# Optimization experiments

Measured on AMD Instinct MI355X. Metric: run time of the kernel, lower is better.

Reference implementation:

```python
import jax, jax.numpy as jnp
import numpy as np

EMBED_DIM = 2048
N_HEADS = 16
HEAD_DIM = EMBED_DIM // N_HEADS


def setup_inputs() -> dict:
    key = jax.random.key(0)
    ks = jax.random.split(key, 5)
    s = 1.0 / np.sqrt(EMBED_DIM)
    x = jax.random.normal(ks[0], (2, 2048, EMBED_DIM), dtype=jnp.float32)
    W_qkv = jax.random.uniform(ks[1], (EMBED_DIM, 3 * EMBED_DIM), jnp.float32, -s, s)
    b_qkv = jax.random.uniform(ks[2], (3 * EMBED_DIM,), jnp.float32, -s, s)
    W_out = jax.random.uniform(ks[3], (EMBED_DIM, EMBED_DIM), jnp.float32, -s, s)
    b_out = jax.random.uniform(ks[4], (EMBED_DIM,), jnp.float32, -s, s)
    return {"x": x, "W_qkv": W_qkv, "b_qkv": b_qkv, "W_out": W_out, "b_out": b_out}


def reference(x, W_qkv, b_qkv, W_out, b_out):
    batch, seq_len, _ = x.shape
    qkv = jnp.einsum('bsd,de->bse', x, W_qkv) + b_qkv
    q, k, v = jnp.split(qkv, 3, axis=-1)
    # [b, h, s, hd]
    def heads(t):
        return t.reshape(batch, seq_len, N_HEADS, HEAD_DIM).transpose(0, 2, 1, 3)
    q, k, v = heads(q), heads(k), heads(v)
    scale = 1.0 / np.sqrt(HEAD_DIM)
    scores = jnp.einsum('bhqd,bhkd->bhqk', q, k) * scale  # [b,h,s,s]
    causal = jnp.tril(jnp.ones((seq_len, seq_len), dtype=bool))
    scores = jnp.where(causal, scores, -jnp.inf)
    attn = jax.nn.softmax(scores, axis=-1)
    out = jnp.einsum('bhqk,bhkd->bhqd', attn, v)
    out = out.transpose(0, 2, 1, 3).reshape(batch, seq_len, EMBED_DIM)
    return jnp.einsum('bsd,de->bse', out, W_out) + b_out
```

## Files before the change

### kernel.cpp

```cpp
#include <hip/hip_runtime.h>
#include <hip/hip_bf16.h>

#define EMBED  2048
#define SEQ    2048
#define BATCH  2
#define NHEADS 16
#define HDIM   128
#define QKVC   (3*EMBED)
#define ROWS   (BATCH*SEQ)

typedef __attribute__((ext_vector_type(8))) short bf16x8;
typedef __attribute__((ext_vector_type(4))) float f32x4;
typedef __attribute__((ext_vector_type(16))) float f32x16;

typedef const __attribute__((address_space(1))) void* gptr1_t;
typedef __attribute__((address_space(3))) void* lptr3_t;

__device__ __forceinline__ void gld16(const unsigned short* g, unsigned short* l) {
  __builtin_amdgcn_global_load_lds((gptr1_t)g, (lptr3_t)l, 16, 0, 0);
}

__device__ __forceinline__ unsigned short f2bf(float f) {
  unsigned int x = __float_as_uint(f);
  unsigned int r = (x + 0x7fffu + ((x >> 16) & 1u)) >> 16;
  return (unsigned short)r;
}

__global__ __launch_bounds__(256)
void prep_kernel(const float* __restrict__ x,
                 const float* __restrict__ Wqkv,
                 const float* __restrict__ Wout,
                 unsigned short* __restrict__ xb,
                 unsigned short* __restrict__ wqkvT,
                 unsigned short* __restrict__ woutT) {
  __shared__ float tile[32][33];
  const int bid = blockIdx.x;
  if (bid < 8192) {
    int i = bid * 256 + threadIdx.x;
    float4 v = reinterpret_cast<const float4*>(x)[i];
    ushort4 o;
    o.x = f2bf(v.x); o.y = f2bf(v.y); o.z = f2bf(v.z); o.w = f2bf(v.w);
    reinterpret_cast<ushort4*>(xb)[i] = o;
    return;
  }
  const float* in; unsigned short* out; int C, bx, by;
  if (bid < 8192 + 12288) {
    int j = bid - 8192;  bx = j % 192; by = j / 192;  in = Wqkv; out = wqkvT; C = QKVC;
  } else {
    int j = bid - 20480; bx = j % 64;  by = j / 64;   in = Wout; out = woutT; C = EMBED;
  }
  const int R = EMBED;
  int tx = threadIdx.x & 31, ty = threadIdx.x >> 5;
  int c0 = bx * 32, r0 = by * 32;
  #pragma unroll
  for (int i = 0; i < 32; i += 8)
    tile[ty + i][tx] = in[(size_t)(r0 + ty + i) * C + c0 + tx];
  __syncthreads();
  #pragma unroll
  for (int i = 0; i < 32; i += 8)
    out[(size_t)(c0 + ty + i) * R + r0 + tx] = f2bf(tile[tx][ty + i]);
}

template<int MODE>
__global__ __launch_bounds__(256)
void gemm_kernel(const unsigned short* __restrict__ A,
                 const unsigned short* __restrict__ BT,
                 const float* __restrict__ bias,
                 unsigned short* __restrict__ outb,
                 unsigned short* __restrict__ vt,
                 float* __restrict__ outf,
                 int M, int N, int K) {
  __shared__ unsigned short As[2 * 128 * 32];
  __shared__ unsigned short Bs[2 * 128 * 32];
  const int t = threadIdx.x;
  const int lane = t & 63, wave = t >> 6;
  const int l31 = lane & 31, hl = lane >> 5;
  const int wm = wave >> 1, wn = wave & 1;
  const int m0 = blockIdx.y * 128, n0 = blockIdx.x * 128;

  f32x16 acc[2][2] = {};

  int aoff[2][4], boff[2][4];
  #pragma unroll
  for (int i = 0; i < 2; ++i) {
    int m = wm * 64 + i * 32 + l31;
    int pm = ((m >> 2) ^ m) & 3;
    int n = wn * 64 + i * 32 + l31;
    int pn = ((n >> 2) ^ n) & 3;
    #pragma unroll
    for (int s4 = 0; s4 < 4; ++s4) {
      int st = s4 >> 1, c = (s4 & 1) * 2 + hl;
      aoff[i][s4] = st * 4096 + (m * 4 + (c ^ pm)) * 8;
      boff[i][s4] = st * 4096 + (n * 4 + (c ^ pn)) * 8;
    }
  }
  int ldso[4];
  const unsigned short* Ag[4];
  const unsigned short* Bg[4];
  #pragma unroll
  for (int i = 0; i < 4; ++i) {
    int cc = i * 256 + t;
    int st = cc >> 9, w = cc & 511;
    int r = w >> 2, s = w & 3;
    int d = s ^ (((r >> 2) ^ r) & 3);
    ldso[i] = st * 4096 + w * 8;
    Ag[i] = A  + (size_t)(m0 + r) * K + st * 32 + d * 8;
    Bg[i] = BT + (size_t)(n0 + r) * K + st * 32 + d * 8;
  }

  for (int k0 = 0; k0 < K; k0 += 64) {
    #pragma unroll
    for (int i = 0; i < 4; ++i) gld16(Ag[i] + k0, &As[ldso[i]]);
    #pragma unroll
    for (int i = 0; i < 4; ++i) gld16(Bg[i] + k0, &Bs[ldso[i]]);
    __syncthreads();
    #pragma unroll
    for (int s4 = 0; s4 < 4; ++s4) {
      bf16x8 a0 = *(const bf16x8*)&As[aoff[0][s4]];
      bf16x8 a1 = *(const bf16x8*)&As[aoff[1][s4]];
      bf16x8 b0 = *(const bf16x8*)&Bs[boff[0][s4]];
      bf16x8 b1 = *(const bf16x8*)&Bs[boff[1][s4]];
      acc[0][0] = __builtin_amdgcn_mfma_f32_32x32x16_bf16(a0, b0, acc[0][0], 0, 0, 0);
      acc[0][1] = __builtin_amdgcn_mfma_f32_32x32x16_bf16(a0, b1, acc[0][1], 0, 0, 0);
      acc[1][0] = __builtin_amdgcn_mfma_f32_32x32x16_bf16(a1, b0, acc[1][0], 0, 0, 0);
      acc[1][1] = __builtin_amdgcn_mfma_f32_32x32x16_bf16(a1, b1, acc[1][1], 0, 0, 0);
    }
    __syncthreads();
  }

  #pragma unroll
  for (int i = 0; i < 2; ++i) {
    int rowb = m0 + wm * 64 + i * 32 + 4 * hl;
    #pragma unroll
    for (int j = 0; j < 2; ++j) {
      int col = n0 + wn * 64 + j * 32 + l31;
      float bv = bias[col];
      if (MODE == 1) {
        #pragma unroll
        for (int g = 0; g < 4; ++g)
          #pragma unroll
          for (int rr = 0; rr < 4; ++rr)
            outf[(size_t)(rowb + 8 * g + rr) * N + col] = acc[i][j][4 * g + rr] + bv;
      } else {
        int hd = col;
        int b = rowb >> 11;
        int sbase = rowb & 2047;
        #pragma unroll
        for (int g = 0; g < 4; ++g) {
          ushort4 w;
          w.x = f2bf(acc[i][j][4 * g + 0] + bv);
          w.y = f2bf(acc[i][j][4 * g + 1] + bv);
          w.z = f2bf(acc[i][j][4 * g + 2] + bv);
          w.w = f2bf(acc[i][j][4 * g + 3] + bv);
          *(ushort4*)&vt[(((size_t)(b << 11) + hd) << 11) + sbase + 8 * g] = w;
        }
      }
    }
  }
}

#define FENCE256 asm volatile("" ::: "memory")
#define BAR256 do { FENCE256; __builtin_amdgcn_s_barrier(); FENCE256; } while (0)

#define STAGE_A256(BUF, H, KT) do { if ((KT) < NT) { \
    gld16(Asrc[0] + (H)*128*K + (KT)*64, &As[BUF][(H)*8192 + sdst0]); \
    gld16(Asrc[1] + (H)*128*K + (KT)*64, &As[BUF][(H)*8192 + sdst1]); } } while (0)
#define STAGE_B256(BUF, H, KT) do { if ((KT) < NT) { \
    gld16(Bsrc[0] + (H)*128*K + (KT)*64, &Bs[BUF][(H)*8192 + sdst0]); \
    gld16(Bsrc[1] + (H)*128*K + (KT)*64, &Bs[BUF][(H)*8192 + sdst1]); } } while (0)

#define READ_A256(BUF, MH) do { _Pragma("unroll") \
  for (int mf = 0; mf < 4; ++mf) { \
    av[mf][0] = *(const bf16x8*)&As[BUF][arow0 + (MH)*4096 + mf*1024 + ck0]; \
    av[mf][1] = *(const bf16x8*)&As[BUF][arow0 + (MH)*4096 + mf*1024 + ck1]; } } while (0)
#define READ_B256(BUF, NH, DST) do { _Pragma("unroll") \
  for (int nf = 0; nf < 2; ++nf) { \
    DST[nf][0] = *(const bf16x8*)&Bs[BUF][brow0 + (NH)*2048 + nf*1024 + ck0]; \
    DST[nf][1] = *(const bf16x8*)&Bs[BUF][brow0 + (NH)*2048 + nf*1024 + ck1]; } } while (0)

#define MFMA_Q256(MH, NH, B_) do { \
  __builtin_amdgcn_s_setprio(1); \
  _Pragma("unroll") \
  for (int mf = 0; mf < 4; ++mf) { \
    _Pragma("unroll") \
    for (int nf = 0; nf < 2; ++nf) { \
      f32x4 c = acc[(MH)*4 + mf][(NH)*2 + nf]; \
      c = __builtin_amdgcn_mfma_f32_16x16x32_bf16(av[mf][0], B_[nf][0], c, 0, 0, 0); \
      c = __builtin_amdgcn_mfma_f32_16x16x32_bf16(av[mf][1], B_[nf][1], c, 0, 0, 0); \
      acc[(MH)*4 + mf][(NH)*2 + nf] = c; } } \
  __builtin_amdgcn_s_setprio(0); } while (0)

#define VMCNT256(LAST) do { \
  if (LAST) asm volatile("s_waitcnt vmcnt(0)" ::: "memory"); \
  else      asm volatile("s_waitcnt vmcnt(4)" ::: "memory"); } while (0)

__global__ __launch_bounds__(512, 2)
void gemm256_kernel(const unsigned short* __restrict__ A,
                    const unsigned short* __restrict__ BT,
                    const float* __restrict__ bias,
                    unsigned short* __restrict__ outb,
                    unsigned short* __restrict__ vt,
                    int M, int N, int K) {
  __shared__ __align__(16) unsigned short As[2][16384];
  __shared__ __align__(16) unsigned short Bs[2][16384];
  const int t = threadIdx.x;
  const int lane = t & 63, wave = t >> 6;
  const int l16 = lane & 15, quad = (lane >> 4) & 3;
  const int wm = wave >> 2, wn = wave & 3;

  const int nwg = (int)gridDim.x;
  int swz = (int)blockIdx.x;
  if ((nwg & 7) == 0) swz = (swz & 7) * (nwg >> 3) + (swz >> 3);
  const int ntiles = N >> 8;
  const int mt = swz / ntiles, nt = swz % ntiles;
  const int m0 = mt << 8, n0 = nt << 8;

  const int NT = K >> 6;
  const int NI = NT >> 1;

  f32x4 acc[8][4] = {};
  bf16x8 av[4][2], bv0[2][2], bv1[2][2];

  const unsigned short* Asrc[2];
  const unsigned short* Bsrc[2];
  int sdst0, sdst1;
  {
    int cc0 = t, cc1 = 512 + t;
    int r0 = cc0 >> 3, c0 = cc0 & 7;
    int r1 = cc1 >> 3, c1 = cc1 & 7;
    Asrc[0] = A  + (size_t)(m0 + r0) * K + ((c0 ^ (r0 & 7)) << 3);
    Asrc[1] = A  + (size_t)(m0 + r1) * K + ((c1 ^ (r1 & 7)) << 3);
    Bsrc[0] = BT + (size_t)(n0 + r0) * K + ((c0 ^ (r0 & 7)) << 3);
    Bsrc[1] = BT + (size_t)(n0 + r1) * K + ((c1 ^ (r1 & 7)) << 3);
    sdst0 = cc0 << 3;
    sdst1 = cc1 << 3;
  }

  const int ck0 = ((quad) ^ (l16 & 7)) << 3;
  const int ck1 = ((4 + quad) ^ (l16 & 7)) << 3;
  const int arow0 = (wm * 128 + l16) * 64;
  const int brow0 = (wn * 64 + l16) * 64;

  STAGE_A256(0, 0, 0); STAGE_A256(0, 1, 0);
  STAGE_B256(0, 0, 0); STAGE_B256(0, 1, 0);
  STAGE_B256(1, 0, 1); STAGE_B256(1, 1, 1);
  asm volatile("s_waitcnt vmcnt(4)" ::: "memory");
  BAR256;

  for (int it = 0; it < NI; ++it) {
    const int kt1 = 2 * it + 1, ktA = 2 * it + 2, ktB = 2 * it + 3;
    const bool last = (it == NI - 1);

    READ_A256(0, 0); READ_B256(0, 0, bv0);
    STAGE_A256(1, 0, kt1);
    BAR256; MFMA_Q256(0, 0, bv0); BAR256;
    READ_B256(0, 1, bv1);
    STAGE_A256(1, 1, kt1);
    BAR256; MFMA_Q256(0, 1, bv1); BAR256;
    READ_A256(0, 1);
    STAGE_B256(0, 0, ktA);
    BAR256; MFMA_Q256(1, 1, bv1); BAR256;
    STAGE_B256(0, 1, ktA);
    BAR256; MFMA_Q256(1, 0, bv0);
    VMCNT256(last);
    BAR256;
    READ_A256(1, 0); READ_B256(1, 0, bv0);
    STAGE_A256(0, 0, ktA);
    BAR256; MFMA_Q256(0, 0, bv0); BAR256;
    READ_B256(1, 1, bv1);
    STAGE_A256(0, 1, ktA);
    BAR256; MFMA_Q256(0, 1, bv1); BAR256;
    READ_A256(1, 1);
    STAGE_B256(1, 0, ktB);
    BAR256; MFMA_Q256(1, 1, bv1); BAR256;
    STAGE_B256(1, 1, ktB);
    BAR256; MFMA_Q256(1, 0, bv0);
    VMCNT256(last);
    BAR256;
  }

  const float scl = (n0 < EMBED) ? (0.08838834764831845f * 1.4426950408889634f) : 1.0f;
  #pragma unroll
  for (int mf = 0; mf < 8; ++mf) {
    const int row = m0 + wm * 128 + (mf >> 2) * 64 + (mf & 3) * 16 + quad * 4;
    #pragma unroll
    for (int nf = 0; nf < 4; ++nf) {
      const int col = n0 + wn * 64 + (nf >> 1) * 32 + (nf & 1) * 16 + l16;
      const float bv = bias[col];
      #pragma unroll
      for (int r = 0; r < 4; ++r)
        outb[(size_t)(row + r) * 4096 + col] = f2bf((acc[mf][nf][r] + bv) * scl);
    }
  }
  (void)vt; (void)M;
}

__global__ __launch_bounds__(512)
void attn_kernel(const unsigned short* __restrict__ qk,
                 const unsigned short* __restrict__ vt,
                 unsigned short* __restrict__ outb) {
  __shared__ unsigned short Ks[2][64 * 128];
  __shared__ unsigned short Vs[2][64 * 128];
  __shared__ unsigned short Ps[8][16 * 72];
  const int t = threadIdx.x;
  const int lane = t & 63, wave = t >> 6;
  const int quad = lane >> 4, l16 = lane & 15;
  const int bh = blockIdx.x;
  const int pair = blockIdx.y;
  const int b = bh >> 4, h = bh & 15;
  const size_t rowbase = (size_t)b * SEQ;
  const int hq = h * HDIM;
  const unsigned short* vbase = vt + ((size_t)bh * HDIM) * SEQ;

  #pragma unroll
  for (int half = 0; half < 2; ++half) {
    const int qt = half ? (15 - pair) : pair;
    const int qw0 = qt * 128 + wave * 16;
    const int jmax = 2 * qt + 1;

    bf16x8 qf[4];
    {
      const unsigned short* qrow = qk + (size_t)(rowbase + qw0 + l16) * 4096 + hq + quad * 8;
      #pragma unroll
      for (int s = 0; s < 4; ++s) qf[s] = *(const bf16x8*)(qrow + s * 32);
    }

    f32x4 o[8] = {};
    float mrow = -1e30f, lrow = 0.f;

    #pragma unroll
    for (int i = 0; i < 2; ++i) {
      int cc = i * 512 + t;
      int kv = cc >> 4, sc = cc & 15;
      int dc = sc ^ (kv & 15);
      gld16(qk + (size_t)(rowbase + kv) * 4096 + EMBED + hq + dc * 8, &Ks[0][cc * 8]);
    }
    #pragma unroll
    for (int i = 0; i < 2; ++i) {
      int cc = i * 512 + t;
      int d = cc >> 3, c = cc & 7;
      int dc = c ^ (d & 7);
      gld16(vbase + (size_t)d * SEQ + dc * 8, &Vs[0][cc * 8]);
    }

    for (int j = 0; j <= jmax; ++j) {
      const int cur = j & 1;
      __syncthreads();

      if (j < jmax) {
        const int kv1 = (j + 1) * 64;
        #pragma unroll
        for (int i = 0; i < 2; ++i) {
          int cc = i * 512 + t;
          int kv = cc >> 4, sc = cc & 15;
          int dc = sc ^ (kv & 15);
          gld16(qk + (size_t)(rowbase + kv1 + kv) * 4096 + EMBED + hq + dc * 8, &Ks[cur ^ 1][cc * 8]);
        }
        #pragma unroll
        for (int i = 0; i < 2; ++i) {
          int cc = i * 512 + t;
          int d = cc >> 3, c = cc & 7;
          int dc = c ^ (d & 7);
          gld16(vbase + (size_t)d * SEQ + kv1 + dc * 8, &Vs[cur ^ 1][cc * 8]);
        }
      }

      const int kv0 = j * 64;
      if (kv0 > qw0 + 15) continue;

      f32x4 sacc[4] = {};
      #pragma unroll
      for (int nb = 0; nb < 4; ++nb) {
        int kvr = nb * 16 + l16;
        #pragma unroll
        for (int ks = 0; ks < 4; ++ks) {
          int dc2 = (ks * 4 + quad) ^ (kvr & 15);
          bf16x8 kb = *(const bf16x8*)&Ks[cur][(kvr * 16 + dc2) * 8];
          sacc[nb] = __builtin_amdgcn_mfma_f32_16x16x32_bf16(kb, qf[ks], sacc[nb], 0, 0, 0);
        }
      }

      float p[4][4];
      float smax = -1e30f;
      if (kv0 + 63 > qw0) {
        const int qg = qw0 + l16;
        #pragma unroll
        for (int nb = 0; nb < 4; ++nb)
          #pragma unroll
          for (int r = 0; r < 4; ++r) {
            float v = sacc[nb][r];
            if ((kv0 + nb * 16 + quad * 4 + r) > qg) v = -1e30f;
            p[nb][r] = v;
            smax = fmaxf(smax, v);
          }
      } else {
        #pragma unroll
        for (int nb = 0; nb < 4; ++nb)
          #pragma unroll
          for (int r = 0; r < 4; ++r) {
            float v = sacc[nb][r];
            p[nb][r] = v;
            smax = fmaxf(smax, v);
          }
      }
      smax = fmaxf(smax, __shfl_xor(smax, 16));
      smax = fmaxf(smax, __shfl_xor(smax, 32));

      const float mold = mrow;
      const unsigned long long grew = __ballot(smax > mold);
      const float mnew = fmaxf(mold, smax);
      mrow = mnew;

      float rs = 0.f;
      #pragma unroll
      for (int nb = 0; nb < 4; ++nb)
        #pragma unroll
        for (int r = 0; r < 4; ++r) {
          float pv = exp2f(p[nb][r] - mnew);
          p[nb][r] = pv;
          rs += pv;
        }
      rs += __shfl_xor(rs, 16);
      rs += __shfl_xor(rs, 32);

      unsigned short* pw = &Ps[wave][0];
      #pragma unroll
      for (int nb = 0; nb < 4; ++nb) {
        __hip_bfloat162 lo = __float22bfloat162_rn(make_float2(p[nb][0], p[nb][1]));
        __hip_bfloat162 hi = __float22bfloat162_rn(make_float2(p[nb][2], p[nb][3]));
        ushort4 w;
        w.x = *(unsigned short*)&lo.x; w.y = *(unsigned short*)&lo.y;
        w.z = *(unsigned short*)&hi.x; w.w = *(unsigned short*)&hi.y;
        *(ushort4*)&pw[l16 * 72 + nb * 16 + quad * 4] = w;
      }

      if (grew) {
        float alpha = exp2f(mold - mnew);
        lrow = lrow * alpha + rs;
        #pragma unroll
        for (int r = 0; r < 4; ++r) {
          float av = __shfl(alpha, quad * 4 + r, 16);
          #pragma unroll
          for (int db = 0; db < 8; ++db) o[db][r] *= av;
        }
      } else {
        lrow += rs;
      }

      asm volatile("s_waitcnt lgkmcnt(0)" ::: "memory");
      bf16x8 pa[2];
      #pragma unroll
      for (int ks2 = 0; ks2 < 2; ++ks2)
        pa[ks2] = *(const bf16x8*)&pw[l16 * 72 + ks2 * 32 + quad * 8];

      #pragma unroll
      for (int db = 0; db < 8; ++db) {
        int d = db * 16 + l16;
        #pragma unroll
        for (int ks2 = 0; ks2 < 2; ++ks2) {
          int dc = (ks2 * 4 + quad) ^ (d & 7);
          bf16x8 vb = *(const bf16x8*)&Vs[cur][(d * 8 + dc) * 8];
          o[db] = __builtin_amdgcn_mfma_f32_16x16x32_bf16(pa[ks2], vb, o[db], 0, 0, 0);
        }
      }
    }

    #pragma unroll
    for (int r = 0; r < 4; ++r) {
      float lr = __shfl(lrow, quad * 4 + r, 16);
      float inv = 1.0f / lr;
      size_t row = rowbase + qw0 + quad * 4 + r;
      #pragma unroll
      for (int db = 0; db < 8; ++db)
        outb[row * EMBED + hq + db * 16 + l16] = f2bf(o[db][r] * inv);
    }
    __syncthreads();
  }
}

extern "C" void kernel_launch(void* const* d_in, const int* in_sizes, int n_in,
                              void* d_out, int out_size, void* d_ws, size_t ws_size,
                              hipStream_t stream) {
  const float* x    = (const float*)d_in[0];
  const float* Wqkv = (const float*)d_in[1];
  const float* bqkv = (const float*)d_in[2];
  const float* Wout = (const float*)d_in[3];
  const float* bout = (const float*)d_in[4];
  float* out = (float*)d_out;

  unsigned short* xb    = (unsigned short*)d_ws;
  unsigned short* wqkvT = xb    + (size_t)ROWS * EMBED;
  unsigned short* woutT = wqkvT + (size_t)EMBED * QKVC;
  unsigned short* qkb   = woutT + (size_t)EMBED * EMBED;
  unsigned short* vtb   = qkb   + (size_t)ROWS * 4096;
  unsigned short* attnb = vtb   + (size_t)32 * HDIM * SEQ;

  prep_kernel<<<dim3(24576), 256, 0, stream>>>(x, Wqkv, Wout, xb, wqkvT, woutT);

  gemm256_kernel<<<dim3((2 * EMBED / 256) * (ROWS / 256)), 512, 0, stream>>>(
      xb, wqkvT, bqkv, qkb, vtb, ROWS, 2 * EMBED, EMBED);

  gemm_kernel<2><<<dim3(EMBED / 128, ROWS / 128), 256, 0, stream>>>(
      xb, wqkvT + (size_t)(2 * EMBED) * EMBED, bqkv + 2 * EMBED,
      nullptr, vtb, nullptr, ROWS, EMBED, EMBED);

  attn_kernel<<<dim3(32, 8), 512, 0, stream>>>(qkb, vtb, attnb);

  gemm_kernel<1><<<dim3(EMBED / 128, ROWS / 128), 256, 0, stream>>>(
      attnb, woutT, bout, nullptr, nullptr, out, ROWS, EMBED, EMBED);
}
```

Measured before the change: 364.3 us.

## Triple-buffer K/V tiles in attention with two-ahead prefetch and partial vmcnt waits

```diff
diff --git a/kernel.cpp b/kernel.cpp
--- a/kernel.cpp
+++ b/kernel.cpp
@@ -299,8 +299,8 @@
 void attn_kernel(const unsigned short* __restrict__ qk,
                  const unsigned short* __restrict__ vt,
                  unsigned short* __restrict__ outb) {
-  __shared__ unsigned short Ks[2][64 * 128];
-  __shared__ unsigned short Vs[2][64 * 128];
+  __shared__ unsigned short Ks[3][64 * 128];
+  __shared__ unsigned short Vs[3][64 * 128];
   __shared__ unsigned short Ps[8][16 * 72];
   const int t = threadIdx.x;
   const int lane = t & 63, wave = t >> 6;
@@ -328,42 +328,38 @@
     f32x4 o[8] = {};
     float mrow = -1e30f, lrow = 0.f;
 
-    #pragma unroll
-    for (int i = 0; i < 2; ++i) {
-      int cc = i * 512 + t;
-      int kv = cc >> 4, sc = cc & 15;
-      int dc = sc ^ (kv & 15);
-      gld16(qk + (size_t)(rowbase + kv) * 4096 + EMBED + hq + dc * 8, &Ks[0][cc * 8]);
-    }
-    #pragma unroll
-    for (int i = 0; i < 2; ++i) {
-      int cc = i * 512 + t;
-      int d = cc >> 3, c = cc & 7;
-      int dc = c ^ (d & 7);
-      gld16(vbase + (size_t)d * SEQ + dc * 8, &Vs[0][cc * 8]);
-    }
-
+    auto STAGEKV = [&](int kt, int bsel) {
+      const int kvb = kt * 64;
+      #pragma unroll
+      for (int i = 0; i < 2; ++i) {
+        int cc = i * 512 + t;
+        int kv = cc >> 4, sc = cc & 15;
+        int dc = sc ^ (kv & 15);
+        gld16(qk + (size_t)(rowbase + kvb + kv) * 4096 + EMBED + hq + dc * 8, &Ks[bsel][cc * 8]);
+      }
+      #pragma unroll
+      for (int i = 0; i < 2; ++i) {
+        int cc = i * 512 + t;
+        int d = cc >> 3, c = cc & 7;
+        int dc = c ^ (d & 7);
+        gld16(vbase + (size_t)d * SEQ + kvb + dc * 8, &Vs[bsel][cc * 8]);
+      }
+    };
+
+    STAGEKV(0, 0);
+    STAGEKV(1, 1);
+
+    int cur = 0, nxt2 = 2;
     for (int j = 0; j <= jmax; ++j) {
-      const int cur = j & 1;
-      __syncthreads();
-
-      if (j < jmax) {
-        const int kv1 = (j + 1) * 64;
-        #pragma unroll
-        for (int i = 0; i < 2; ++i) {
-          int cc = i * 512 + t;
-          int kv = cc >> 4, sc = cc & 15;
-          int dc = sc ^ (kv & 15);
-          gld16(qk + (size_t)(rowbase + kv1 + kv) * 4096 + EMBED + hq + dc * 8, &Ks[cur ^ 1][cc * 8]);
-        }
-        #pragma unroll
-        for (int i = 0; i < 2; ++i) {
-          int cc = i * 512 + t;
-          int d = cc >> 3, c = cc & 7;
-          int dc = c ^ (d & 7);
-          gld16(vbase + (size_t)d * SEQ + kv1 + dc * 8, &Vs[cur ^ 1][cc * 8]);
-        }
-      }
+      if (j < jmax) { asm volatile("s_waitcnt vmcnt(4)" ::: "memory"); }
+      else          { asm volatile("s_waitcnt vmcnt(0)" ::: "memory"); }
+      FENCE256; __builtin_amdgcn_s_barrier(); FENCE256;
+
+      if (j + 2 <= jmax) STAGEKV(j + 2, nxt2);
+
+      const int buf = cur;
+      cur  = (cur  == 2) ? 0 : cur  + 1;
+      nxt2 = (nxt2 == 2) ? 0 : nxt2 + 1;
 
       const int kv0 = j * 64;
       if (kv0 > qw0 + 15) continue;
@@ -375,7 +371,7 @@
         #pragma unroll
         for (int ks = 0; ks < 4; ++ks) {
           int dc2 = (ks * 4 + quad) ^ (kvr & 15);
-          bf16x8 kb = *(const bf16x8*)&Ks[cur][(kvr * 16 + dc2) * 8];
+          bf16x8 kb = *(const bf16x8*)&Ks[buf][(kvr * 16 + dc2) * 8];
           sacc[nb] = __builtin_amdgcn_mfma_f32_16x16x32_bf16(kb, qf[ks], sacc[nb], 0, 0, 0);
         }
       }
@@ -459,7 +455,7 @@
         #pragma unroll
         for (int ks2 = 0; ks2 < 2; ++ks2) {
           int dc = (ks2 * 4 + quad) ^ (d & 7);
-          bf16x8 vb = *(const bf16x8*)&Vs[cur][(d * 8 + dc) * 8];
+          bf16x8 vb = *(const bf16x8*)&Vs[buf][(d * 8 + dc) * 8];
           o[db] = __builtin_amdgcn_mfma_f32_16x16x32_bf16(pa[ks2], vb, o[db], 0, 0, 0);
         }
       }
```

Result: no change. 360.6 us (-1.0%).
